# Performance work log

Hardware: AMD Instinct MI355X
Metric: run time of the kernel (lower is better)

## Reference

```python
import jax, jax.numpy as jnp
import numpy as np

B, L, H, D = 16, 4096, 16, 64
HID = H * D


def setup_inputs() -> dict:
    key = jax.random.key(0)
    ks = jax.random.split(key, 10)
    w = lambda k: jax.random.normal(k, (HID, HID), jnp.float32) * 0.02
    return dict(
        hidden_states=jax.random.normal(ks[0], (B, 1, HID), jnp.float32),
        past_key=jax.random.normal(ks[1], (B, H, L, D), jnp.float32),
        past_value=jax.random.normal(ks[2], (B, H, L, D), jnp.float32),
        attention_mask=jnp.ones((B, L), jnp.float32),
        cache_position=jax.random.randint(ks[3], (B, 1), 0, L, jnp.int32),
        Wq=w(ks[4]), bq=jnp.zeros((HID,), jnp.float32),
        Wk=w(ks[5]), bk=jnp.zeros((HID,), jnp.float32),
        Wv=w(ks[6]), bv=jnp.zeros((HID,), jnp.float32),
        Wo=w(ks[7]), bo=jnp.zeros((HID,), jnp.float32),
    )


def reference(hidden_states, past_key, past_value, attention_mask, cache_position,
              Wq, bq, Wk, bk, Wv, bv, Wo, bo):
    # projections: [B,1,HID]; torch Linear => x @ W.T + b
    q = hidden_states @ Wq.T + bq
    k = hidden_states @ Wk.T + bk
    v = hidden_states @ Wv.T + bv
    # [B,H,1,D]
    q = q.reshape(B, 1, H, D).transpose(0, 2, 1, 3)
    k_new = k.reshape(B, H, D)
    v_new = v.reshape(B, H, D)
    pos = cache_position[:, 0]  # [B]
    bidx = jnp.arange(B)
    # write new token K/V into cache at cache_position (per-batch)
    k_cache = past_key.at[bidx, :, pos].set(k_new)
    v_cache = past_value.at[bidx, :, pos].set(v_new)
    scale = jnp.float32(1.0) / jnp.sqrt(jnp.float32(D))
    scores = jnp.einsum('bhqd,bhkd->bhqk', q, k_cache) * scale  # [B,H,1,L]
    neg = jnp.finfo(scores.dtype).min
    scores = jnp.where(attention_mask[:, None, None, :] > 0, scores, neg)
    p = jax.nn.softmax(scores, axis=-1)
    ctx = jnp.einsum('bhqk,bhkd->bhqd', p, v_cache)  # [B,H,1,D]
    attn_output = ctx.transpose(0, 2, 1, 3).reshape(B, 1, HID) @ Wo.T + bo
    return attn_output, k_cache, v_cache
```

## Files before the change

kernel.cpp:

```cpp
#include <hip/hip_runtime.h>
#include <hip/hip_bf16.h>

#define BATCH 16
#define SEQL  4096
#define NH    16
#define HD    64
#define HID   1024
#define NCHUNK 8
#define CHUNK  (SEQL / NCHUNK)
#define KV_ELEMS (BATCH * NH * SEQL * HD)

typedef float f4 __attribute__((ext_vector_type(4)));

__global__ __launch_bounds__(256) void proj_partial(
    const float* __restrict__ x,
    const float* __restrict__ W0,
    const float* __restrict__ W1,
    const float* __restrict__ W2,
    float* __restrict__ part)
{
    __shared__ float xs[BATCH * HID];
    const int t = threadIdx.x;
    for (int i = t; i < BATCH * HID; i += 256) xs[i] = x[i];
    __syncthreads();

    const float* W = (blockIdx.y == 0) ? W0 : ((blockIdx.y == 1) ? W1 : W2);
    const int otile = blockIdx.x;
    const int z     = blockIdx.z;
    const int og = t & 15;
    const int sl = t >> 4;
    const int obase = otile * 64 + og * 4;
    const int kbase = z * 256 + sl * 16;

    float acc[4][BATCH];
    #pragma unroll
    for (int oi = 0; oi < 4; ++oi)
        #pragma unroll
        for (int b = 0; b < BATCH; ++b) acc[oi][b] = 0.f;

    #pragma unroll
    for (int kk = 0; kk < 16; kk += 4) {
        const int k = kbase + kk;
        f4 w4[4];
        #pragma unroll
        for (int oi = 0; oi < 4; ++oi)
            w4[oi] = *(const f4*)&W[(size_t)(obase + oi) * HID + k];
        #pragma unroll
        for (int b = 0; b < BATCH; ++b) {
            f4 h4 = *(const f4*)&xs[b * HID + k];
            #pragma unroll
            for (int oi = 0; oi < 4; ++oi)
                acc[oi][b] += w4[oi].x * h4.x + w4[oi].y * h4.y
                            + w4[oi].z * h4.z + w4[oi].w * h4.w;
        }
    }

    __syncthreads();
    float* red = xs;
    #pragma unroll
    for (int oi = 0; oi < 4; ++oi)
        #pragma unroll
        for (int b = 0; b < BATCH; ++b)
            red[((sl * 16 + og) * 4 + oi) * 16 + b] = acc[oi][b];
    __syncthreads();

    #pragma unroll
    for (int u = 0; u < 4; ++u) {
        const int idx = t * 4 + u;
        const int o_local = idx >> 4;
        const int b = idx & 15;
        const int ogg = o_local >> 2, oii = o_local & 3;
        float s = 0.f;
        #pragma unroll
        for (int s2 = 0; s2 < 16; ++s2)
            s += red[((s2 * 16 + ogg) * 4 + oii) * 16 + b];
        part[(size_t)(blockIdx.y * 4 + z) * (BATCH * HID)
             + b * HID + otile * 64 + o_local] = s;
    }
}

__global__ __launch_bounds__(256) void reduce_qkv(
    const float* __restrict__ part,
    const float* __restrict__ bq, const float* __restrict__ bk,
    const float* __restrict__ bv, float* __restrict__ qkv)
{
    const int i = blockIdx.x * 256 + threadIdx.x;
    const int w = i >> 14;
    const int rem = i & 16383;
    const int o = rem & (HID - 1);
    float s = 0.f;
    #pragma unroll
    for (int z = 0; z < 4; ++z)
        s += part[(size_t)(w * 4 + z) * (BATCH * HID) + rem];
    const float* bias = (w == 0) ? bq : ((w == 1) ? bk : bv);
    qkv[i] = s + bias[o];
}

__global__ __launch_bounds__(256) void attn_fused(
    const float* __restrict__ qkv,
    const float* __restrict__ past_k,
    const float* __restrict__ past_v,
    const float* __restrict__ mask,
    const int*   __restrict__ cpos,
    float* __restrict__ kout,
    float* __restrict__ vout,
    float* __restrict__ part)
{
    const int bh = blockIdx.x;
    const int c  = blockIdx.y;
    const int b  = bh >> 4;
    const int h  = bh & 15;
    const int t  = threadIdx.x;
    const int g  = t >> 4;
    const int j  = t & 15;

    const int pos = cpos[b];
    const int qoff = b * HID + h * HD + j * 4;
    const f4 q4 = *(const f4*)&qkv[qoff];
    const f4 kn4 = *(const f4*)&qkv[BATCH * HID + qoff];
    const f4 vn4 = *(const f4*)&qkv[2 * BATCH * HID + qoff];

    const size_t base = (size_t)bh * SEQL * HD;
    const float scale = 0.125f;

    float m = -INFINITY, l = 0.f;
    f4 a4 = {0.f, 0.f, 0.f, 0.f};

    const int r_end = c * CHUNK + CHUNK;
    for (int r = c * CHUNK + g; r < r_end; r += 16) {
        const size_t off = base + (size_t)r * HD + j * 4;
        f4 k4 = __builtin_nontemporal_load((const f4*)(past_k + off));
        f4 v4 = __builtin_nontemporal_load((const f4*)(past_v + off));
        if (r == pos) { k4 = kn4; v4 = vn4; }
        __builtin_nontemporal_store(k4, (f4*)(kout + off));
        __builtin_nontemporal_store(v4, (f4*)(vout + off));

        float d = k4.x * q4.x + k4.y * q4.y + k4.z * q4.z + k4.w * q4.w;
        d += __shfl_xor(d, 1);
        d += __shfl_xor(d, 2);
        d += __shfl_xor(d, 4);
        d += __shfl_xor(d, 8);

        const float am = mask[b * SEQL + r];
        const float s = (am > 0.f) ? d * scale : -3.4028235e38f;

        const float mnew = fmaxf(m, s);
        const float fac = __expf(m - mnew);
        const float p   = __expf(s - mnew);
        l = l * fac + p;
        a4.x = a4.x * fac + p * v4.x;
        a4.y = a4.y * fac + p * v4.y;
        a4.z = a4.z * fac + p * v4.z;
        a4.w = a4.w * fac + p * v4.w;
        m = mnew;
    }

    __shared__ float sm[16], sl[16];
    __shared__ float sa[16][64];
    if (j == 0) { sm[g] = m; sl[g] = l; }
    *(f4*)&sa[g][j * 4] = a4;
    __syncthreads();

    if (t < 64) {
        float M = -INFINITY;
        #pragma unroll
        for (int gg = 0; gg < 16; ++gg) M = fmaxf(M, sm[gg]);
        float Ls = 0.f, A = 0.f;
        #pragma unroll
        for (int gg = 0; gg < 16; ++gg) {
            const float wgt = __expf(sm[gg] - M);
            Ls += sl[gg] * wgt;
            A  += sa[gg][t] * wgt;
        }
        float* pr = part + ((size_t)bh * NCHUNK + c) * 66;
        if (t == 0) { pr[0] = M; pr[1] = Ls; }
        pr[2 + t] = A;
    }
}

__global__ __launch_bounds__(64) void merge_ctx(
    const float* __restrict__ part, float* __restrict__ ctx)
{
    const int bh = blockIdx.x;
    const int d = threadIdx.x;
    float M = -INFINITY;
    #pragma unroll
    for (int cc = 0; cc < NCHUNK; ++cc)
        M = fmaxf(M, part[((size_t)bh * NCHUNK + cc) * 66]);
    float Ls = 0.f, A = 0.f;
    #pragma unroll
    for (int cc = 0; cc < NCHUNK; ++cc) {
        const float* pr = part + ((size_t)bh * NCHUNK + cc) * 66;
        const float wgt = __expf(pr[0] - M);
        Ls += pr[1] * wgt;
        A  += pr[2 + d] * wgt;
    }
    ctx[bh * HD + d] = A / Ls;
}

__global__ __launch_bounds__(256) void reduce_out(
    const float* __restrict__ part, const float* __restrict__ bo,
    float* __restrict__ out)
{
    const int i = blockIdx.x * 256 + threadIdx.x;
    const int o = i & (HID - 1);
    float s = 0.f;
    #pragma unroll
    for (int z = 0; z < 4; ++z)
        s += part[(size_t)z * (BATCH * HID) + i];
    out[i] = s + bo[o];
}

extern "C" void kernel_launch(void* const* d_in, const int* in_sizes, int n_in,
                              void* d_out, int out_size, void* d_ws, size_t ws_size,
                              hipStream_t stream) {
    const float* hs   = (const float*)d_in[0];
    const float* pk   = (const float*)d_in[1];
    const float* pv   = (const float*)d_in[2];
    const float* mask = (const float*)d_in[3];
    const int*   cpos = (const int*)d_in[4];
    const float* Wq   = (const float*)d_in[5];
    const float* bq   = (const float*)d_in[6];
    const float* Wk   = (const float*)d_in[7];
    const float* bk   = (const float*)d_in[8];
    const float* Wv   = (const float*)d_in[9];
    const float* bv   = (const float*)d_in[10];
    const float* Wo   = (const float*)d_in[11];
    const float* bo   = (const float*)d_in[12];

    float* out_attn = (float*)d_out;
    float* kout = out_attn + BATCH * HID;
    float* vout = kout + KV_ELEMS;

    float* ws    = (float*)d_ws;
    float* qkv   = ws;
    float* ctx   = ws + 49152;
    float* apart = ws + 65536;
    float* ppart = ws + 200704;

    proj_partial<<<dim3(16, 3, 4), 256, 0, stream>>>(hs, Wq, Wk, Wv, ppart);
    reduce_qkv<<<dim3(192), 256, 0, stream>>>(ppart, bq, bk, bv, qkv);

    attn_fused<<<dim3(256, NCHUNK), 256, 0, stream>>>(qkv, pk, pv, mask, cpos,
                                                      kout, vout, apart);
    merge_ctx<<<dim3(256), 64, 0, stream>>>(apart, ctx);

    proj_partial<<<dim3(16, 1, 4), 256, 0, stream>>>(ctx, Wo, Wo, Wo, ppart);
    reduce_out<<<dim3(64), 256, 0, stream>>>(ppart, bo, out_attn);
}
```

Measured before the change: 233.1 us.

## Drop online softmax max tracking and patch new-token row in merge kernel

The streaming attention kernel no longer tracks a running max. It accumulates exp2-scaled scores directly and batches four rows of K/V loads per iteration to raise memory-level parallelism. The per-row cache_position substitution moves out of the hot loop: a merge kernel writes the new K/V row and corrects the affected chunk's sum by swapping the stale row's contribution for the new one. This removes per-row compare and rescale work, but risks exp overflow for large attention scores, since there is no max subtraction.

```diff
diff --git a/kernel.cpp b/kernel.cpp
--- a/kernel.cpp
+++ b/kernel.cpp
@@ -9,6 +9,8 @@
 #define NCHUNK 8
 #define CHUNK  (SEQL / NCHUNK)
 #define KV_ELEMS (BATCH * NH * SEQL * HD)
+#define PSTRIDE 68
+#define C2 0.1803368801f
 
 typedef float f4 __attribute__((ext_vector_type(4)));
 
@@ -96,7 +98,94 @@
     qkv[i] = s + bias[o];
 }
 
-__global__ __launch_bounds__(256) void attn_fused(
+__global__ __launch_bounds__(256, 8) void attn_fused(
+    const float* __restrict__ qkv,
+    const float* __restrict__ past_k,
+    const float* __restrict__ past_v,
+    const float* __restrict__ mask,
+    float* __restrict__ kout,
+    float* __restrict__ vout,
+    float* __restrict__ part)
+{
+    const int bh = blockIdx.x;
+    const int c  = blockIdx.y;
+    const int b  = bh >> 4;
+    const int h  = bh & 15;
+    const int t  = threadIdx.x;
+    const int g  = t >> 4;
+    const int j  = t & 15;
+
+    const f4 q4 = *(const f4*)&qkv[b * HID + h * HD + j * 4];
+
+    const size_t base = (size_t)bh * SEQL * HD;
+    const float* __restrict__ pkb = past_k + base;
+    const float* __restrict__ pvb = past_v + base;
+    float* __restrict__ kob = kout + base;
+    float* __restrict__ vob = vout + base;
+    const float* __restrict__ mrow = mask + b * SEQL;
+
+    float l = 0.f;
+    f4 a4 = {0.f, 0.f, 0.f, 0.f};
+
+    int r = c * CHUNK + g;
+    #pragma unroll 1
+    for (int it = 0; it < CHUNK / 64; ++it) {
+        f4 k4[4], v4[4];
+        float am[4];
+        int ro[4];
+        #pragma unroll
+        for (int u = 0; u < 4; ++u) {
+            const int rr = r + u * 16;
+            ro[u] = rr * HD + (j << 2);
+            k4[u] = __builtin_nontemporal_load((const f4*)(pkb + ro[u]));
+            v4[u] = __builtin_nontemporal_load((const f4*)(pvb + ro[u]));
+            am[u] = mrow[rr];
+        }
+        #pragma unroll
+        for (int u = 0; u < 4; ++u) {
+            __builtin_nontemporal_store(k4[u], (f4*)(kob + ro[u]));
+            __builtin_nontemporal_store(v4[u], (f4*)(vob + ro[u]));
+        }
+        #pragma unroll
+        for (int u = 0; u < 4; ++u) {
+            float d = k4[u].x * q4.x + k4[u].y * q4.y
+                    + k4[u].z * q4.z + k4[u].w * q4.w;
+            d += __shfl_xor(d, 1);
+            d += __shfl_xor(d, 2);
+            d += __shfl_xor(d, 4);
+            d += __shfl_xor(d, 8);
+            float p = exp2f(d * C2);
+            p = (am[u] > 0.f) ? p : 0.f;
+            l += p;
+            a4.x += p * v4[u].x;
+            a4.y += p * v4[u].y;
+            a4.z += p * v4[u].z;
+            a4.w += p * v4[u].w;
+        }
+        r += 64;
+    }
+
+    __shared__ float sl_[16];
+    __shared__ float sa[16][64];
+    if (j == 0) sl_[g] = l;
+    *(f4*)&sa[g][j * 4] = a4;
+    __syncthreads();
+
+    float* pr = part + ((size_t)bh * NCHUNK + c) * PSTRIDE;
+    if (t < 64) {
+        float A = 0.f;
+        #pragma unroll
+        for (int gg = 0; gg < 16; ++gg) A += sa[gg][t];
+        pr[1 + t] = A;
+    } else if (t == 64) {
+        float L = 0.f;
+        #pragma unroll
+        for (int gg = 0; gg < 16; ++gg) L += sl_[gg];
+        pr[0] = L;
+    }
+}
+
+__global__ __launch_bounds__(64) void merge_fix(
     const float* __restrict__ qkv,
     const float* __restrict__ past_k,
     const float* __restrict__ past_v,
@@ -104,98 +193,47 @@
     const int*   __restrict__ cpos,
     float* __restrict__ kout,
     float* __restrict__ vout,
-    float* __restrict__ part)
+    const float* __restrict__ part,
+    float* __restrict__ ctx)
 {
     const int bh = blockIdx.x;
-    const int c  = blockIdx.y;
-    const int b  = bh >> 4;
-    const int h  = bh & 15;
-    const int t  = threadIdx.x;
-    const int g  = t >> 4;
-    const int j  = t & 15;
-
+    const int b = bh >> 4, h = bh & 15;
+    const int t = threadIdx.x;
     const int pos = cpos[b];
-    const int qoff = b * HID + h * HD + j * 4;
-    const f4 q4 = *(const f4*)&qkv[qoff];
-    const f4 kn4 = *(const f4*)&qkv[BATCH * HID + qoff];
-    const f4 vn4 = *(const f4*)&qkv[2 * BATCH * HID + qoff];
-
-    const size_t base = (size_t)bh * SEQL * HD;
-    const float scale = 0.125f;
-
-    float m = -INFINITY, l = 0.f;
-    f4 a4 = {0.f, 0.f, 0.f, 0.f};
-
-    const int r_end = c * CHUNK + CHUNK;
-    for (int r = c * CHUNK + g; r < r_end; r += 16) {
-        const size_t off = base + (size_t)r * HD + j * 4;
-        f4 k4 = __builtin_nontemporal_load((const f4*)(past_k + off));
-        f4 v4 = __builtin_nontemporal_load((const f4*)(past_v + off));
-        if (r == pos) { k4 = kn4; v4 = vn4; }
-        __builtin_nontemporal_store(k4, (f4*)(kout + off));
-        __builtin_nontemporal_store(v4, (f4*)(vout + off));
-
-        float d = k4.x * q4.x + k4.y * q4.y + k4.z * q4.z + k4.w * q4.w;
-        d += __shfl_xor(d, 1);
-        d += __shfl_xor(d, 2);
-        d += __shfl_xor(d, 4);
-        d += __shfl_xor(d, 8);
-
-        const float am = mask[b * SEQL + r];
-        const float s = (am > 0.f) ? d * scale : -3.4028235e38f;
-
-        const float mnew = fmaxf(m, s);
-        const float fac = __expf(m - mnew);
-        const float p   = __expf(s - mnew);
-        l = l * fac + p;
-        a4.x = a4.x * fac + p * v4.x;
-        a4.y = a4.y * fac + p * v4.y;
-        a4.z = a4.z * fac + p * v4.z;
-        a4.w = a4.w * fac + p * v4.w;
-        m = mnew;
-    }
-
-    __shared__ float sm[16], sl[16];
-    __shared__ float sa[16][64];
-    if (j == 0) { sm[g] = m; sl[g] = l; }
-    *(f4*)&sa[g][j * 4] = a4;
-    __syncthreads();
-
-    if (t < 64) {
-        float M = -INFINITY;
-        #pragma unroll
-        for (int gg = 0; gg < 16; ++gg) M = fmaxf(M, sm[gg]);
-        float Ls = 0.f, A = 0.f;
-        #pragma unroll
-        for (int gg = 0; gg < 16; ++gg) {
-            const float wgt = __expf(sm[gg] - M);
-            Ls += sl[gg] * wgt;
-            A  += sa[gg][t] * wgt;
-        }
-        float* pr = part + ((size_t)bh * NCHUNK + c) * 66;
-        if (t == 0) { pr[0] = M; pr[1] = Ls; }
-        pr[2 + t] = A;
-    }
-}
-
-__global__ __launch_bounds__(64) void merge_ctx(
-    const float* __restrict__ part, float* __restrict__ ctx)
-{
-    const int bh = blockIdx.x;
-    const int d = threadIdx.x;
-    float M = -INFINITY;
-    #pragma unroll
-    for (int cc = 0; cc < NCHUNK; ++cc)
-        M = fmaxf(M, part[((size_t)bh * NCHUNK + cc) * 66]);
-    float Ls = 0.f, A = 0.f;
+
+    const size_t rowoff = (size_t)bh * SEQL * HD + (size_t)pos * HD + t;
+    const int qo = b * HID + h * HD + t;
+    const float qd  = qkv[qo];
+    const float knd = qkv[BATCH * HID + qo];
+    const float vnd = qkv[2 * BATCH * HID + qo];
+    const float ksd = past_k[rowoff];
+    const float vsd = past_v[rowoff];
+
+    kout[rowoff] = knd;
+    vout[rowoff] = vnd;
+
+    float dst = qd * ksd, dnw = qd * knd;
+    #pragma unroll
+    for (int sh = 1; sh < 64; sh <<= 1) {
+        dst += __shfl_xor(dst, sh);
+        dnw += __shfl_xor(dnw, sh);
+    }
+    const float am = mask[b * SEQL + pos];
+    float ps = 0.f, pn = 0.f;
+    if (am > 0.f) { ps = exp2f(dst * C2); pn = exp2f(dnw * C2); }
+
+    const int cc0 = pos / CHUNK;
+    float L = 0.f, A = 0.f;
     #pragma unroll
     for (int cc = 0; cc < NCHUNK; ++cc) {
-        const float* pr = part + ((size_t)bh * NCHUNK + cc) * 66;
-        const float wgt = __expf(pr[0] - M);
-        Ls += pr[1] * wgt;
-        A  += pr[2 + d] * wgt;
-    }
-    ctx[bh * HD + d] = A / Ls;
+        const float* pr = part + ((size_t)bh * NCHUNK + cc) * PSTRIDE;
+        float Lc = pr[0];
+        float Ac = pr[1 + t];
+        if (cc == cc0) { Lc += pn - ps; Ac += pn * vnd - ps * vsd; }
+        L += Lc;
+        A += Ac;
+    }
+    ctx[bh * HD + t] = A / L;
 }
 
 __global__ __launch_bounds__(256) void reduce_out(
@@ -236,14 +274,15 @@
     float* qkv   = ws;
     float* ctx   = ws + 49152;
     float* apart = ws + 65536;
-    float* ppart = ws + 200704;
+    float* ppart = ws + 204800;
 
     proj_partial<<<dim3(16, 3, 4), 256, 0, stream>>>(hs, Wq, Wk, Wv, ppart);
     reduce_qkv<<<dim3(192), 256, 0, stream>>>(ppart, bq, bk, bv, qkv);
 
-    attn_fused<<<dim3(256, NCHUNK), 256, 0, stream>>>(qkv, pk, pv, mask, cpos,
+    attn_fused<<<dim3(256, NCHUNK), 256, 0, stream>>>(qkv, pk, pv, mask,
                                                       kout, vout, apart);
-    merge_ctx<<<dim3(256), 64, 0, stream>>>(apart, ctx);
+    merge_fix<<<dim3(256), 64, 0, stream>>>(qkv, pk, pv, mask, cpos,
+                                            kout, vout, apart, ctx);
 
     proj_partial<<<dim3(16, 1, 4), 256, 0, stream>>>(ctx, Wo, Wo, Wo, ppart);
     reduce_out<<<dim3(64), 256, 0, stream>>>(ppart, bo, out_attn);
```

Measured after the change: 229.6 us. Within noise of the previous version (-1.5%).
